# Kernel optimization log

Hardware: AMD Instinct MI355X
Metric: run time of the kernel (lower is better)

The kernel has to match this reference:

```python
import jax, jax.numpy as jnp
import numpy as np

H = 8      # num_heads
DH = 80    # head_dim = embed_dim // num_heads


def setup_inputs() -> dict:
    key = jax.random.key(0)
    ks = jax.random.split(key, 7)
    B, T, S = 8, 4096, 77
    hidden, embed, ctx = 640, 640, 768
    sc_h = 1.0 / np.sqrt(hidden)
    sc_c = 1.0 / np.sqrt(ctx)
    sc_e = 1.0 / np.sqrt(embed)
    return {
        "tokens": jax.random.normal(ks[0], (B, T, hidden), jnp.float32),
        "context": jax.random.normal(ks[1], (B, S, ctx), jnp.float32),
        "Wq": jax.random.normal(ks[2], (hidden, embed), jnp.float32) * sc_h,
        "Wk": jax.random.normal(ks[3], (ctx, embed), jnp.float32) * sc_c,
        "Wv": jax.random.normal(ks[4], (ctx, embed), jnp.float32) * sc_c,
        "Wo": jax.random.normal(ks[5], (embed, hidden), jnp.float32) * sc_e,
        "bo": jnp.zeros((hidden,), jnp.float32),
    }


def reference(tokens, context, Wq, Wk, Wv, Wo, bo):
    B, T, _ = tokens.shape
    S = context.shape[1]
    Q = (tokens @ Wq).reshape(B, T, H, DH)    # B T H D
    K = (context @ Wk).reshape(B, S, H, DH)   # B S H D
    V = (context @ Wv).reshape(B, S, H, DH)
    scores = jnp.einsum('bthd,bshd->bhts', Q, K) / jnp.sqrt(jnp.float32(DH))
    attn = jax.nn.softmax(scores, axis=-1)    # B H T S
    ctx_vecs = jnp.einsum('bhts,bshd->bthd', attn, V).reshape(B, T, H * DH)
    return ctx_vecs @ Wo + bo
```

## Files before the change

kernel.cpp:

```cpp
#include <hip/hip_runtime.h>
#include <hip/hip_bf16.h>
#include <hip/hip_fp16.h>

typedef __attribute__((ext_vector_type(4))) float f32x4;
typedef __attribute__((ext_vector_type(8))) _Float16 f16x8;
typedef __attribute__((ext_vector_type(8))) unsigned short u16x8;

__device__ __forceinline__ unsigned short f2h(float f) {
    _Float16 h = (_Float16)f;
    return __builtin_bit_cast(unsigned short, h);
}

#define GLOAD_LDS16(gp, lp) __builtin_amdgcn_global_load_lds( \
    (const __attribute__((address_space(1))) void*)(gp), \
    (__attribute__((address_space(3))) void*)(lp), 16, 0, 0)
#define PRIO1() __builtin_amdgcn_s_setprio(1)
#define PRIO0() __builtin_amdgcn_s_setprio(0)

__global__ void cvt_kernel(const float* __restrict__ in, ushort* __restrict__ out, int n4) {
    int stride = gridDim.x * blockDim.x;
    for (int i = blockIdx.x * blockDim.x + threadIdx.x; i < n4; i += stride) {
        float4 v = ((const float4*)in)[i];
        ushort4 o;
        o.x = f2h(v.x); o.y = f2h(v.y); o.z = f2h(v.z); o.w = f2h(v.w);
        ((ushort4*)out)[i] = o;
    }
}

__global__ void transpose_cvt2(const float* __restrict__ Wk, const float* __restrict__ Wv,
                               ushort* __restrict__ WkvT) {
    __shared__ float tile[32][33];
    const int z = blockIdx.z;
    const float* src = z ? Wv : Wk;
    ushort* dst = WkvT + (size_t)z * 640 * 768;
    const int R = 768, C = 640;
    int tx = threadIdx.x, ty = threadIdx.y;
    int c = blockIdx.x * 32 + tx;
    int r0 = blockIdx.y * 32;
#pragma unroll
    for (int i = ty; i < 32; i += 8) {
        int r = r0 + i;
        tile[i][tx] = (r < R && c < C) ? src[(size_t)r * C + c] : 0.f;
    }
    __syncthreads();
    int rr = r0 + tx;
    int c0 = blockIdx.x * 32;
#pragma unroll
    for (int i = ty; i < 32; i += 8) {
        int cc = c0 + i;
        if (cc < C && rr < R) dst[(size_t)cc * R + rr] = f2h(tile[tx][i]);
    }
}

__global__ void pack_wfrag(const float* __restrict__ W, ushort* __restrict__ WF) {
    int g = blockIdx.x * 256 + threadIdx.x;
    if (g >= 51200) return;
    int lane = g & 63;
    int fi = (g >> 6) % 10;
    int kt = ((g >> 6) / 10) % 10;
    int h  = (g >> 6) / 100;
    int ni = fi >> 1, kk = fi & 1;
    int n  = h * 80 + ni * 16 + (lane & 15);
    int k0 = kt * 64 + kk * 32 + (lane >> 4) * 8;
    u16x8 o;
#pragma unroll
    for (int e = 0; e < 8; ++e) o[e] = f2h(W[(size_t)(k0 + e) * 640 + n]);
    *(u16x8*)&WF[(size_t)g * 8] = o;
}

__global__ void pack_kvfrag(const ushort* __restrict__ KVb,
                            ushort* __restrict__ KF, ushort* __restrict__ VF) {
    int g = blockIdx.x * 256 + threadIdx.x;
    if (g >= 61440) return;
    int lane = g & 63;
    int fi = (g >> 6) % 15;
    int bh = (g >> 6) / 15;
    int b = bh >> 3, h = bh & 7;
    int ni = fi / 3, kk = fi % 3;
    int l15 = lane & 15, lhi = lane >> 4;
    int sr = ni * 16 + l15; if (sr > 76) sr = 76;
    int d0 = kk * 32 + lhi * 8;
    u16x8 ko, vo;
#pragma unroll
    for (int e = 0; e < 8; ++e)
        ko[e] = KVb[((size_t)b * 77 + sr) * 1280 + h * 80 + d0 + e];
    int dv = ni * 16 + l15;
    int s0 = kk * 32 + lhi * 8;
#pragma unroll
    for (int e = 0; e < 8; ++e) {
        int s = s0 + e;
        vo[e] = (s < 77) ? KVb[((size_t)b * 77 + s) * 1280 + 640 + h * 80 + dv] : (ushort)0;
    }
    *(u16x8*)&KF[(size_t)g * 8] = ko;
    *(u16x8*)&VF[(size_t)g * 8] = vo;
}

template<int OUT_F16, int HAS_BIAS>
__global__ __launch_bounds__(256) void gemm_bt(
    const ushort* __restrict__ A, const ushort* __restrict__ Bt,
    void* __restrict__ C, const float* __restrict__ bias,
    int M, int N, int K)
{
    __shared__ ushort As[128 * 64];
    __shared__ ushort Bs[128 * 64];
    const int tid = threadIdx.x;
    const int lane = tid & 63;
    const int w = tid >> 6;
    const int wr = (w >> 1) * 64, wc = (w & 1) * 64;
    const int m0 = blockIdx.x * 128, n0 = blockIdx.y * 128;
    const int l15 = lane & 15, lhi = lane >> 4;

    f32x4 acc[4][4] = {};

    for (int k0 = 0; k0 < K; k0 += 64) {
        __syncthreads();
#pragma unroll
        for (int i = 0; i < 4; ++i) {
            int c = i * 256 + tid;
            int m = m0 + (c >> 3);
            if (m > M - 1) m = M - 1;
            GLOAD_LDS16(A + (size_t)m * K + k0 + (c & 7) * 8, &As[c * 8]);
        }
#pragma unroll
        for (int i = 0; i < 4; ++i) {
            int c = i * 256 + tid;
            GLOAD_LDS16(Bt + (size_t)(n0 + (c >> 3)) * K + k0 + (c & 7) * 8, &Bs[c * 8]);
        }
        __syncthreads();
#pragma unroll
        for (int kk = 0; kk < 2; ++kk) {
            f16x8 af[4], bfr[4];
#pragma unroll
            for (int mi = 0; mi < 4; ++mi)
                af[mi] = *(const f16x8*)&As[(wr + mi * 16 + l15) * 64 + kk * 32 + lhi * 8];
#pragma unroll
            for (int ni = 0; ni < 4; ++ni)
                bfr[ni] = *(const f16x8*)&Bs[(wc + ni * 16 + l15) * 64 + kk * 32 + lhi * 8];
#pragma unroll
            for (int mi = 0; mi < 4; ++mi)
#pragma unroll
                for (int ni = 0; ni < 4; ++ni)
                    acc[mi][ni] = __builtin_amdgcn_mfma_f32_16x16x32_f16(
                        af[mi], bfr[ni], acc[mi][ni], 0, 0, 0);
        }
    }

#pragma unroll
    for (int mi = 0; mi < 4; ++mi)
#pragma unroll
        for (int ni = 0; ni < 4; ++ni)
#pragma unroll
            for (int r = 0; r < 4; ++r) {
                int row = m0 + wr + mi * 16 + lhi * 4 + r;
                int col = n0 + wc + ni * 16 + l15;
                if (row < M) {
                    float v = acc[mi][ni][r];
                    if (HAS_BIAS) v += bias[col];
                    if (OUT_F16) ((ushort*)C)[(size_t)row * N + col] = f2h(v);
                    else         ((float*)C)[(size_t)row * N + col] = v;
                }
            }
}

__global__ __launch_bounds__(512, 2) void fused_attn(
    const float* __restrict__ tokens, const ushort* __restrict__ WqF,
    const ushort* __restrict__ KF, const ushort* __restrict__ VF,
    const ushort* __restrict__ WoF, const float* __restrict__ bo,
    float* __restrict__ out)
{
    __shared__ __align__(16) ushort lds[20480];
    const int tid = threadIdx.x;
    const int lane = tid & 63;
    const int w = tid >> 6;
    const int l15 = lane & 15, lhi = lane >> 4;
    const int tt = blockIdx.x, b = blockIdx.y;
    const size_t rowbase = (size_t)b * 4096 + (size_t)tt * 32;

    const ushort* WqFb = WqF + (size_t)w * 10 * 5120;
    const ushort* WoFb = WoF + (size_t)w * 10 * 5120;
    const ushort* KFb  = KF + (size_t)(b * 8 + w) * 15 * 512;
    const ushort* VFb  = VF + (size_t)(b * 8 + w) * 15 * 512;

    {
        const int srow = tid >> 4;
        const int c16  = tid & 15;
        const float* tbase = tokens + (rowbase + srow) * 640 + c16 * 8;
        float4 sA[5], sB[5];
#pragma unroll
        for (int i = 0; i < 5; ++i) {
            sA[i] = ((const float4*)(tbase + i * 128))[0];
            sB[i] = ((const float4*)(tbase + i * 128))[1];
        }
#pragma unroll
        for (int i = 0; i < 5; ++i) {
            int slot = i * 16 + c16;
            int phys = (slot & ~7) | ((slot ^ srow) & 7);
            u16x8 o;
            o[0]=f2h(sA[i].x); o[1]=f2h(sA[i].y); o[2]=f2h(sA[i].z); o[3]=f2h(sA[i].w);
            o[4]=f2h(sB[i].x); o[5]=f2h(sB[i].y); o[6]=f2h(sB[i].z); o[7]=f2h(sB[i].w);
            *(u16x8*)&lds[srow * 640 + phys * 8] = o;
        }
    }
    f16x8 PE[5], PO[5];
#pragma unroll
    for (int f = 0; f < 5; ++f)
        PE[f] = *(const f16x8*)(WqFb + (f * 2) * 512 + lane * 8);
    __syncthreads();

    f32x4 qacc[2][5] = {};
#define GHALF(ACC, PC, PN, WB, KT, KK, NKT, NKK, DOPF) do { \
    if (DOPF) { \
        _Pragma("unroll") for (int f = 0; f < 5; ++f) \
            (PN)[f] = *(const f16x8*)((WB) + (size_t)(NKT) * 5120 + (f * 2 + (NKK)) * 512 + lane * 8); \
    } \
    f16x8 af[2]; \
    _Pragma("unroll") for (int mi = 0; mi < 2; ++mi) { \
        int row_ = mi * 16 + l15; \
        af[mi] = *(const f16x8*)&lds[row_ * 640 + ((KT) * 8 + (((KK) * 4 + lhi) ^ (row_ & 7))) * 8]; \
    } \
    PRIO1(); \
    _Pragma("unroll") for (int mi = 0; mi < 2; ++mi) \
    _Pragma("unroll") for (int ni = 0; ni < 5; ++ni) \
        (ACC)[mi][ni] = __builtin_amdgcn_mfma_f32_16x16x32_f16(af[mi], (PC)[ni], (ACC)[mi][ni], 0, 0, 0); \
    PRIO0(); \
} while (0)

    for (int kt = 0; kt < 10; ++kt) {
        GHALF(qacc, PE, PO, WqFb, kt, 0, kt, 1, 1);
        GHALF(qacc, PO, PE, WqFb, kt, 1, kt + 1, 0, kt < 9);
    }
    __syncthreads();

    const int qoff = w * 2560;
#pragma unroll
    for (int mi = 0; mi < 2; ++mi)
#pragma unroll
        for (int ni = 0; ni < 5; ++ni)
#pragma unroll
            for (int r = 0; r < 4; ++r)
                lds[qoff + (mi*16 + lhi*4 + r)*80 + ni*16 + l15] = f2h(qacc[mi][ni][r]);
    __builtin_amdgcn_sched_barrier(0);

    const f16x8 zf = {};
    f32x4 sa[2][5] = {};
#define ATT_KK(ACC, PC, PN, FB, KK, NKK, DOPF) do { \
    if (DOPF) { \
        _Pragma("unroll") for (int f = 0; f < 5; ++f) \
            (PN)[f] = *(const f16x8*)((FB) + (f * 3 + (NKK)) * 512 + lane * 8); \
    } \
    f16x8 aq[2]; \
    const int kcol = ((KK) < 2) ? ((KK)*32 + lhi*8) : (64 + (lhi & 1)*8); \
    _Pragma("unroll") for (int mi = 0; mi < 2; ++mi) { \
        aq[mi] = *(const f16x8*)&lds[qoff + (mi*16 + l15)*80 + kcol]; \
        if ((KK) == 2 && lhi >= 2) aq[mi] = zf; \
    } \
    PRIO1(); \
    _Pragma("unroll") for (int mi = 0; mi < 2; ++mi) \
    _Pragma("unroll") for (int ni = 0; ni < 5; ++ni) \
        (ACC)[mi][ni] = __builtin_amdgcn_mfma_f32_16x16x32_f16(aq[mi], (PC)[ni], (ACC)[mi][ni], 0, 0, 0); \
    PRIO0(); \
} while (0)

#pragma unroll
    for (int f = 0; f < 5; ++f)
        PE[f] = *(const f16x8*)(KFb + (f * 3) * 512 + lane * 8);
    ATT_KK(sa, PE, PO, KFb, 0, 1, 1);
    ATT_KK(sa, PO, PE, KFb, 1, 2, 1);
    ATT_KK(sa, PE, PO, KFb, 2, 0, 0);
    __builtin_amdgcn_sched_barrier(0);

    const float sc = 0.11180339887498949f;
#pragma unroll
    for (int mi = 0; mi < 2; ++mi)
#pragma unroll
        for (int r = 0; r < 4; ++r) {
            float v0 = sa[mi][0][r]*sc, v1 = sa[mi][1][r]*sc, v2 = sa[mi][2][r]*sc,
                  v3 = sa[mi][3][r]*sc, v4 = sa[mi][4][r]*sc;
            bool ok4 = l15 < 13;
            float mx = fmaxf(fmaxf(v0, v1), fmaxf(v2, v3));
            if (ok4) mx = fmaxf(mx, v4);
#pragma unroll
            for (int off = 1; off < 16; off <<= 1) mx = fmaxf(mx, __shfl_xor(mx, off, 16));
            float p0 = __expf(v0-mx), p1 = __expf(v1-mx), p2 = __expf(v2-mx), p3 = __expf(v3-mx);
            float p4 = ok4 ? __expf(v4-mx) : 0.f;
            float sm = p0+p1+p2+p3+p4;
#pragma unroll
            for (int off = 1; off < 16; off <<= 1) sm += __shfl_xor(sm, off, 16);
            float inv = 1.f / sm;
            int row = mi*16 + lhi*4 + r;
            lds[qoff + row*80 + 0*16 + l15] = f2h(p0*inv);
            lds[qoff + row*80 + 1*16 + l15] = f2h(p1*inv);
            lds[qoff + row*80 + 2*16 + l15] = f2h(p2*inv);
            lds[qoff + row*80 + 3*16 + l15] = f2h(p3*inv);
            lds[qoff + row*80 + 4*16 + l15] = f2h(p4*inv);
        }
    __builtin_amdgcn_sched_barrier(0);

    f32x4 oa[2][5] = {};
#pragma unroll
    for (int f = 0; f < 5; ++f)
        PE[f] = *(const f16x8*)(VFb + (f * 3) * 512 + lane * 8);
    ATT_KK(oa, PE, PO, VFb, 0, 1, 1);
    ATT_KK(oa, PO, PE, VFb, 1, 2, 1);
    ATT_KK(oa, PE, PO, VFb, 2, 0, 0);
#undef ATT_KK
    __syncthreads();

#pragma unroll
    for (int mi = 0; mi < 2; ++mi)
#pragma unroll
        for (int ni = 0; ni < 5; ++ni)
#pragma unroll
            for (int r = 0; r < 4; ++r) {
                int row = mi*16 + lhi*4 + r;
                int col = w*80 + ni*16 + l15;
                int slot = col >> 3;
                int phys = (slot & ~7) | ((slot ^ row) & 7);
                lds[row*640 + phys*8 + (col & 7)] = f2h(oa[mi][ni][r]);
            }
    __syncthreads();

    f32x4 cacc[2][5] = {};
#pragma unroll
    for (int f = 0; f < 5; ++f)
        PE[f] = *(const f16x8*)(WoFb + (f * 2) * 512 + lane * 8);
    for (int kt = 0; kt < 10; ++kt) {
        GHALF(cacc, PE, PO, WoFb, kt, 0, kt, 1, 1);
        GHALF(cacc, PO, PE, WoFb, kt, 1, kt + 1, 0, kt < 9);
    }
#undef GHALF

#pragma unroll
    for (int ni = 0; ni < 5; ++ni) {
        int col = w*80 + ni*16 + l15;
        float bvl = bo[col];
#pragma unroll
        for (int mi = 0; mi < 2; ++mi)
#pragma unroll
            for (int r = 0; r < 4; ++r)
                out[(rowbase + mi*16 + lhi*4 + r) * 640 + col] = cacc[mi][ni][r] + bvl;
    }
}

extern "C" void kernel_launch(void* const* d_in, const int* in_sizes, int n_in,
                              void* d_out, int out_size, void* d_ws, size_t ws_size,
                              hipStream_t stream) {
    (void)in_sizes; (void)n_in; (void)out_size; (void)ws_size;
    const float* tokens  = (const float*)d_in[0];
    const float* context = (const float*)d_in[1];
    const float* Wq = (const float*)d_in[2];
    const float* Wk = (const float*)d_in[3];
    const float* Wv = (const float*)d_in[4];
    const float* Wo = (const float*)d_in[5];
    const float* bo = (const float*)d_in[6];
    float* out = (float*)d_out;

    ushort* ws   = (ushort*)d_ws;
    ushort* ctx16 = ws;
    ushort* WkvT = ctx16 + (size_t)616 * 768;
    ushort* KVb  = WkvT + (size_t)1280 * 768;
    ushort* WqF  = KVb  + (size_t)616 * 1280;
    ushort* WoF  = WqF  + (size_t)640 * 640;
    ushort* KF   = WoF  + (size_t)640 * 640;
    ushort* VF   = KF   + (size_t)61440 * 8;

    cvt_kernel<<<462, 256, 0, stream>>>(context, ctx16, 616 * 768 / 4);
    transpose_cvt2<<<dim3(20, 24, 2), dim3(32, 8), 0, stream>>>(Wk, Wv, WkvT);
    pack_wfrag<<<200, 256, 0, stream>>>(Wq, WqF);
    pack_wfrag<<<200, 256, 0, stream>>>(Wo, WoF);
    gemm_bt<1, 0><<<dim3(5, 10), 256, 0, stream>>>(ctx16, WkvT, KVb, nullptr, 616, 1280, 768);
    pack_kvfrag<<<240, 256, 0, stream>>>(KVb, KF, VF);
    fused_attn<<<dim3(128, 8), 512, 0, stream>>>(tokens, WqF, KF, VF, WoF, bo, out);
}
```

Baseline: 129.8 us.

## Enlarge fused attention tile to 128 rows with double-buffered token staging

Each block of the fused attention kernel now handles 128 token rows instead of 32, so each weight fragment loaded from global memory (Wq, K, V, Wo) is reused across four times as many MFMA tiles. The token tile is no longer staged all at once. It streams through LDS in 64-column chunks with a two-buffer ping-pong, and the next chunk's global load overlaps the current chunk's MFMAs. The cost is a much larger accumulator footprint (8x5 f32x4 per array), LDS raised to 160KB, occupancy bound lowered to one block per CU, and a grid of only 256 blocks. That risks register spills and under-filling the GPU.

```diff
diff --git a/kernel.cpp b/kernel.cpp
--- a/kernel.cpp
+++ b/kernel.cpp
@@ -162,44 +162,53 @@
             }
 }
 
-__global__ __launch_bounds__(512, 2) void fused_attn(
+__global__ __launch_bounds__(512, 1) void fused_attn(
     const float* __restrict__ tokens, const ushort* __restrict__ WqF,
     const ushort* __restrict__ KF, const ushort* __restrict__ VF,
     const ushort* __restrict__ WoF, const float* __restrict__ bo,
     float* __restrict__ out)
 {
-    __shared__ __align__(16) ushort lds[20480];
+    __shared__ __align__(16) ushort lds[81920];
     const int tid = threadIdx.x;
     const int lane = tid & 63;
     const int w = tid >> 6;
     const int l15 = lane & 15, lhi = lane >> 4;
     const int tt = blockIdx.x, b = blockIdx.y;
-    const size_t rowbase = (size_t)b * 4096 + (size_t)tt * 32;
+    const size_t rowbase = (size_t)b * 4096 + (size_t)tt * 128;
 
     const ushort* WqFb = WqF + (size_t)w * 10 * 5120;
     const ushort* WoFb = WoF + (size_t)w * 10 * 5120;
     const ushort* KFb  = KF + (size_t)(b * 8 + w) * 15 * 512;
     const ushort* VFb  = VF + (size_t)(b * 8 + w) * 15 * 512;
 
+    const int r0s = tid >> 3;
+    const int r1s = r0s + 64;
+    const int s0s = tid & 7;
+    const int d0s = r0s * 64 + (s0s ^ (r0s & 7)) * 8;
+    const int d1s = r1s * 64 + (s0s ^ (r1s & 7)) * 8;
+
+#define STAGE_LOAD(C, A0, B0, A1, B1) do { \
+    const float* p0_ = tokens + (rowbase + r0s) * 640 + (C) * 64 + s0s * 8; \
+    const float* p1_ = tokens + (rowbase + r1s) * 640 + (C) * 64 + s0s * 8; \
+    A0 = ((const float4*)p0_)[0]; B0 = ((const float4*)p0_)[1]; \
+    A1 = ((const float4*)p1_)[0]; B1 = ((const float4*)p1_)[1]; \
+} while (0)
+#define STAGE_WRITE(BUF, A0, B0, A1, B1) do { \
+    u16x8 o0_, o1_; \
+    o0_[0]=f2h(A0.x); o0_[1]=f2h(A0.y); o0_[2]=f2h(A0.z); o0_[3]=f2h(A0.w); \
+    o0_[4]=f2h(B0.x); o0_[5]=f2h(B0.y); o0_[6]=f2h(B0.z); o0_[7]=f2h(B0.w); \
+    o1_[0]=f2h(A1.x); o1_[1]=f2h(A1.y); o1_[2]=f2h(A1.z); o1_[3]=f2h(A1.w); \
+    o1_[4]=f2h(B1.x); o1_[5]=f2h(B1.y); o1_[6]=f2h(B1.z); o1_[7]=f2h(B1.w); \
+    *(u16x8*)&lds[(BUF) * 8192 + d0s] = o0_; \
+    *(u16x8*)&lds[(BUF) * 8192 + d1s] = o1_; \
+} while (0)
+
     {
-        const int srow = tid >> 4;
-        const int c16  = tid & 15;
-        const float* tbase = tokens + (rowbase + srow) * 640 + c16 * 8;
-        float4 sA[5], sB[5];
-#pragma unroll
-        for (int i = 0; i < 5; ++i) {
-            sA[i] = ((const float4*)(tbase + i * 128))[0];
-            sB[i] = ((const float4*)(tbase + i * 128))[1];
-        }
-#pragma unroll
-        for (int i = 0; i < 5; ++i) {
-            int slot = i * 16 + c16;
-            int phys = (slot & ~7) | ((slot ^ srow) & 7);
-            u16x8 o;
-            o[0]=f2h(sA[i].x); o[1]=f2h(sA[i].y); o[2]=f2h(sA[i].z); o[3]=f2h(sA[i].w);
-            o[4]=f2h(sB[i].x); o[5]=f2h(sB[i].y); o[6]=f2h(sB[i].z); o[7]=f2h(sB[i].w);
-            *(u16x8*)&lds[srow * 640 + phys * 8] = o;
-        }
+        float4 a0, b0, a1, b1, c0, d0, c1, d1;
+        STAGE_LOAD(0, a0, b0, a1, b1);
+        STAGE_LOAD(1, c0, d0, c1, d1);
+        STAGE_WRITE(0, a0, b0, a1, b1);
+        STAGE_WRITE(1, c0, d0, c1, d1);
     }
     f16x8 PE[5], PO[5];
 #pragma unroll
@@ -207,33 +216,35 @@
         PE[f] = *(const f16x8*)(WqFb + (f * 2) * 512 + lane * 8);
     __syncthreads();
 
-    f32x4 qacc[2][5] = {};
-#define GHALF(ACC, PC, PN, WB, KT, KK, NKT, NKK, DOPF) do { \
+    f32x4 qacc[8][5] = {};
+#define MHALF(ACC, PC, PN, WB, CURB, RSTR, SBASE, KK, NKT, NKK, DOPF) do { \
     if (DOPF) { \
         _Pragma("unroll") for (int f = 0; f < 5; ++f) \
             (PN)[f] = *(const f16x8*)((WB) + (size_t)(NKT) * 5120 + (f * 2 + (NKK)) * 512 + lane * 8); \
     } \
-    f16x8 af[2]; \
-    _Pragma("unroll") for (int mi = 0; mi < 2; ++mi) { \
+    PRIO1(); \
+    _Pragma("unroll") for (int mi = 0; mi < 8; ++mi) { \
         int row_ = mi * 16 + l15; \
-        af[mi] = *(const f16x8*)&lds[row_ * 640 + ((KT) * 8 + (((KK) * 4 + lhi) ^ (row_ & 7))) * 8]; \
+        f16x8 a_ = *(const f16x8*)&lds[(CURB) + row_ * (RSTR) + ((SBASE) + (((KK) * 4 + lhi) ^ (row_ & 7))) * 8]; \
+        _Pragma("unroll") for (int ni = 0; ni < 5; ++ni) \
+            (ACC)[mi][ni] = __builtin_amdgcn_mfma_f32_16x16x32_f16(a_, (PC)[ni], (ACC)[mi][ni], 0, 0, 0); \
     } \
-    PRIO1(); \
-    _Pragma("unroll") for (int mi = 0; mi < 2; ++mi) \
-    _Pragma("unroll") for (int ni = 0; ni < 5; ++ni) \
-        (ACC)[mi][ni] = __builtin_amdgcn_mfma_f32_16x16x32_f16(af[mi], (PC)[ni], (ACC)[mi][ni], 0, 0, 0); \
     PRIO0(); \
 } while (0)
 
     for (int kt = 0; kt < 10; ++kt) {
-        GHALF(qacc, PE, PO, WqFb, kt, 0, kt, 1, 1);
-        GHALF(qacc, PO, PE, WqFb, kt, 1, kt + 1, 0, kt < 9);
-    }
-    __syncthreads();
-
-    const int qoff = w * 2560;
-#pragma unroll
-    for (int mi = 0; mi < 2; ++mi)
+        const int curb = (kt & 1) * 8192;
+        float4 a0, b0, a1, b1;
+        if (kt < 8) STAGE_LOAD(kt + 2, a0, b0, a1, b1);
+        MHALF(qacc, PE, PO, WqFb, curb, 64, 0, 0, kt, 1, 1);
+        MHALF(qacc, PO, PE, WqFb, curb, 64, 0, 1, kt + 1, 0, kt < 9);
+        __syncthreads();
+        if (kt < 8) STAGE_WRITE(kt & 1, a0, b0, a1, b1);
+    }
+
+    const int qoff = w * 10240;
+#pragma unroll
+    for (int mi = 0; mi < 8; ++mi)
 #pragma unroll
         for (int ni = 0; ni < 5; ++ni)
 #pragma unroll
@@ -242,22 +253,20 @@
     __builtin_amdgcn_sched_barrier(0);
 
     const f16x8 zf = {};
-    f32x4 sa[2][5] = {};
+    f32x4 sa[8][5] = {};
 #define ATT_KK(ACC, PC, PN, FB, KK, NKK, DOPF) do { \
     if (DOPF) { \
         _Pragma("unroll") for (int f = 0; f < 5; ++f) \
             (PN)[f] = *(const f16x8*)((FB) + (f * 3 + (NKK)) * 512 + lane * 8); \
     } \
-    f16x8 aq[2]; \
     const int kcol = ((KK) < 2) ? ((KK)*32 + lhi*8) : (64 + (lhi & 1)*8); \
-    _Pragma("unroll") for (int mi = 0; mi < 2; ++mi) { \
-        aq[mi] = *(const f16x8*)&lds[qoff + (mi*16 + l15)*80 + kcol]; \
-        if ((KK) == 2 && lhi >= 2) aq[mi] = zf; \
+    PRIO1(); \
+    _Pragma("unroll") for (int mi = 0; mi < 8; ++mi) { \
+        f16x8 aq_ = *(const f16x8*)&lds[qoff + (mi*16 + l15)*80 + kcol]; \
+        if ((KK) == 2 && lhi >= 2) aq_ = zf; \
+        _Pragma("unroll") for (int ni = 0; ni < 5; ++ni) \
+            (ACC)[mi][ni] = __builtin_amdgcn_mfma_f32_16x16x32_f16(aq_, (PC)[ni], (ACC)[mi][ni], 0, 0, 0); \
     } \
-    PRIO1(); \
-    _Pragma("unroll") for (int mi = 0; mi < 2; ++mi) \
-    _Pragma("unroll") for (int ni = 0; ni < 5; ++ni) \
-        (ACC)[mi][ni] = __builtin_amdgcn_mfma_f32_16x16x32_f16(aq[mi], (PC)[ni], (ACC)[mi][ni], 0, 0, 0); \
     PRIO0(); \
 } while (0)
 
@@ -271,7 +280,7 @@
 
     const float sc = 0.11180339887498949f;
 #pragma unroll
-    for (int mi = 0; mi < 2; ++mi)
+    for (int mi = 0; mi < 8; ++mi)
 #pragma unroll
         for (int r = 0; r < 4; ++r) {
             float v0 = sa[mi][0][r]*sc, v1 = sa[mi][1][r]*sc, v2 = sa[mi][2][r]*sc,
@@ -296,7 +305,7 @@
         }
     __builtin_amdgcn_sched_barrier(0);
 
-    f32x4 oa[2][5] = {};
+    f32x4 oa[8][5] = {};
 #pragma unroll
     for (int f = 0; f < 5; ++f)
         PE[f] = *(const f16x8*)(VFb + (f * 3) * 512 + lane * 8);
@@ -307,7 +316,7 @@
     __syncthreads();
 
 #pragma unroll
-    for (int mi = 0; mi < 2; ++mi)
+    for (int mi = 0; mi < 8; ++mi)
 #pragma unroll
         for (int ni = 0; ni < 5; ++ni)
 #pragma unroll
@@ -320,26 +329,28 @@
             }
     __syncthreads();
 
-    f32x4 cacc[2][5] = {};
+    f32x4 cacc[8][5] = {};
 #pragma unroll
     for (int f = 0; f < 5; ++f)
         PE[f] = *(const f16x8*)(WoFb + (f * 2) * 512 + lane * 8);
     for (int kt = 0; kt < 10; ++kt) {
-        GHALF(cacc, PE, PO, WoFb, kt, 0, kt, 1, 1);
-        GHALF(cacc, PO, PE, WoFb, kt, 1, kt + 1, 0, kt < 9);
-    }
-#undef GHALF
+        MHALF(cacc, PE, PO, WoFb, 0, 640, kt * 8, 0, kt, 1, 1);
+        MHALF(cacc, PO, PE, WoFb, 0, 640, kt * 8, 1, kt + 1, 0, kt < 9);
+    }
+#undef MHALF
 
 #pragma unroll
     for (int ni = 0; ni < 5; ++ni) {
         int col = w*80 + ni*16 + l15;
         float bvl = bo[col];
 #pragma unroll
-        for (int mi = 0; mi < 2; ++mi)
+        for (int mi = 0; mi < 8; ++mi)
 #pragma unroll
             for (int r = 0; r < 4; ++r)
                 out[(rowbase + mi*16 + lhi*4 + r) * 640 + col] = cacc[mi][ni][r] + bvl;
     }
+#undef STAGE_LOAD
+#undef STAGE_WRITE
 }
 
 extern "C" void kernel_launch(void* const* d_in, const int* in_sizes, int n_in,
@@ -370,5 +381,5 @@
     pack_wfrag<<<200, 256, 0, stream>>>(Wo, WoF);
     gemm_bt<1, 0><<<dim3(5, 10), 256, 0, stream>>>(ctx16, WkvT, KVb, nullptr, 616, 1280, 768);
     pack_kvfrag<<<240, 256, 0, stream>>>(KVb, KF, VF);
-    fused_attn<<<dim3(128, 8), 512, 0, stream>>>(tokens, WqF, KF, VF, WoF, bo, out);
-}
+    fused_attn<<<dim3(32, 8), 512, 0, stream>>>(tokens, WqF, KF, VF, WoF, bo, out);
+}
```

Result: faster. 118.5 us (-8.8%).
